# Performance work log

Hardware: AMD Instinct MI355X
Metric: run time of the kernel (lower is better)

## Reference

```python
import jax, jax.numpy as jnp
import numpy as np

B, P_LEN, Q_LEN, HID = 8, 2048, 1024, 1024


def setup_inputs() -> dict:
    key = jax.random.key(0)
    k1, k2, k3, k4 = jax.random.split(key, 4)
    k = jax.random.normal(k1, (B, P_LEN, HID), dtype=jnp.float32)
    q = jax.random.normal(k2, (B, Q_LEN, HID), dtype=jnp.float32)
    # q_mask: True = pad token. All-valid mask (no pads) to avoid NaN rows.
    q_mask = jnp.zeros((B, Q_LEN), dtype=bool)
    # Xavier-normal-initialized Linear weights, shape [out, in] as in torch.
    std = float(np.sqrt(2.0 / (HID + HID)))
    Wk = jax.random.normal(k3, (HID, HID), dtype=jnp.float32) * std
    Wq = jax.random.normal(k4, (HID, HID), dtype=jnp.float32) * std
    return {"k": k, "q": q, "q_mask": q_mask, "Wk": Wk, "Wq": Wq}


def reference(k, q, q_mask, Wk, Wq):
    # relu-projected keys/queries (Linear has no bias)
    p_key = jax.nn.relu(jnp.einsum('bpd,hd->bph', k, Wk))   # [B, p_len, hid]
    q_key = jax.nn.relu(jnp.einsum('bqd,hd->bqh', q, Wq))   # [B, q_len, hid]
    scores = jnp.einsum('bph,bqh->bpq', p_key, q_key)        # [B, p_len, q_len]
    scores = jnp.where(q_mask[:, None, :], -jnp.inf, scores)
    alphas = jax.nn.softmax(scores, axis=-1)                 # [B, p_len, q_len]
    ctx = jnp.einsum('bpq,bqd->bpd', alphas, q)              # [B, p_len, q_dim]
    return ctx, alphas
```

## Files before the change

### kernel.cpp

```cpp
#include <hip/hip_runtime.h>
#include <hip/hip_bf16.h>
#include <math.h>


typedef _Float16 v8h __attribute__((ext_vector_type(8)));
typedef _Float16 v4h __attribute__((ext_vector_type(4)));
typedef float v4f __attribute__((ext_vector_type(4)));

#define AS1C(p) ((const __attribute__((address_space(1))) void*)(p))
#define AS3(p)  ((__attribute__((address_space(3))) void*)(p))

__global__ __launch_bounds__(256) void gemm_nt_f16_128(
    const _Float16* __restrict__ A, const _Float16* __restrict__ B,
    float* __restrict__ Cf, _Float16* __restrict__ Ch,
    const _Float16* __restrict__ B2, _Float16* __restrict__ Ch2, int mtSplit,
    int N, int K, int Mtiles, int Ntiles,
    long long sA, long long sB, long long sC, int relu)
{
  extern __shared__ _Float16 lds[];

  const int nwg = gridDim.x;
  const int cpx = nwg >> 3;
  const int bid = (blockIdx.x & 7) * cpx + (blockIdx.x >> 3);
  const int nt  = bid % Ntiles;
  const int mt  = (bid / Ntiles) % Mtiles;
  const int bz  = bid / (Mtiles * Ntiles);

  A += (long long)bz * sA;

  const _Float16* Bp = B;
  _Float16* Chp = Ch;
  int m0c = mt * 128;
  if (mt >= mtSplit) { Bp = B2; Chp = Ch2; m0c = (mt - mtSplit) * 128; }
  Bp += (long long)bz * sB;

  const int m0g = mt * 128;
  const int n0  = nt * 128;
  const int t   = threadIdx.x;
  const int l   = t & 63;
  const int w   = t >> 6;
  const int wm  = (w >> 1) * 64;
  const int wn  = (w & 1) * 64;
  const int fr  = l & 15;
  const int fq  = l >> 4;
  const int r3  = fr & 7;
  const int sa0 = (fq ^ r3) * 8;
  const int sa1 = ((4 + fq) ^ r3) * 8;

  const int trow = t >> 3;
  const int tswz = ((t & 7) ^ (trow & 7)) * 8;

  const _Float16* Ast = A  + (long long)(m0g + trow) * K + tswz;
  const _Float16* Bst = Bp + (long long)(n0  + trow) * K + tswz;

  v4f acc[4][4];
#pragma unroll
  for (int i = 0; i < 4; ++i)
#pragma unroll
    for (int j = 0; j < 4; ++j)
      acc[i][j] = (v4f){0.f, 0.f, 0.f, 0.f};

  const int NT = K >> 6;

#define STAGE(kt) do {                                                                   \
    _Float16* s_ = lds + (((kt) & 1) << 14);                                             \
    const long long ko_ = (long long)((kt) << 6);                                        \
    __builtin_amdgcn_global_load_lds(AS1C(Ast + ko_),               AS3(s_ +        t * 8), 16, 0, 0); \
    __builtin_amdgcn_global_load_lds(AS1C(Ast + 32LL * K + ko_),    AS3(s_ + 2048 + t * 8), 16, 0, 0); \
    __builtin_amdgcn_global_load_lds(AS1C(Ast + 64LL * K + ko_),    AS3(s_ + 4096 + t * 8), 16, 0, 0); \
    __builtin_amdgcn_global_load_lds(AS1C(Ast + 96LL * K + ko_),    AS3(s_ + 6144 + t * 8), 16, 0, 0); \
    __builtin_amdgcn_global_load_lds(AS1C(Bst + ko_),               AS3(s_ + 8192 + t * 8), 16, 0, 0); \
    __builtin_amdgcn_global_load_lds(AS1C(Bst + 32LL * K + ko_),    AS3(s_ + 10240 + t * 8), 16, 0, 0); \
    __builtin_amdgcn_global_load_lds(AS1C(Bst + 64LL * K + ko_),    AS3(s_ + 12288 + t * 8), 16, 0, 0); \
    __builtin_amdgcn_global_load_lds(AS1C(Bst + 96LL * K + ko_),    AS3(s_ + 14336 + t * 8), 16, 0, 0); \
  } while (0)

  STAGE(0);

  for (int kt = 0; kt < NT; ++kt) {
    if (kt + 1 < NT) {
      STAGE(kt + 1);
      asm volatile("s_waitcnt vmcnt(8)" ::: "memory");
    } else {
      asm volatile("s_waitcnt vmcnt(0)" ::: "memory");
    }
    __builtin_amdgcn_sched_barrier(0);
    __builtin_amdgcn_s_barrier();
    asm volatile("" ::: "memory");

    const _Float16* Ab = lds + ((kt & 1) << 14);
    const _Float16* Bb = Ab + 8192;

    v8h a0[4], a1[4], b0[4], b1[4];

#pragma unroll
    for (int i = 0; i < 4; ++i) {
      a0[i] = *(const v8h*)&Ab[(wm + i * 16 + fr) * 64 + sa0];
      a1[i] = *(const v8h*)&Ab[(wm + i * 16 + fr) * 64 + sa1];
    }
#pragma unroll
    for (int j = 0; j < 2; ++j) {
      b0[j] = *(const v8h*)&Bb[(wn + j * 16 + fr) * 64 + sa0];
      b1[j] = *(const v8h*)&Bb[(wn + j * 16 + fr) * 64 + sa1];
    }
    __builtin_amdgcn_s_setprio(1);
#pragma unroll
    for (int i = 0; i < 4; ++i)
#pragma unroll
      for (int j = 0; j < 2; ++j) {
        acc[i][j] = __builtin_amdgcn_mfma_f32_16x16x32_f16(a0[i], b0[j], acc[i][j], 0, 0, 0);
        acc[i][j] = __builtin_amdgcn_mfma_f32_16x16x32_f16(a1[i], b1[j], acc[i][j], 0, 0, 0);
      }
    __builtin_amdgcn_s_setprio(0);

#pragma unroll
    for (int j = 2; j < 4; ++j) {
      b0[j] = *(const v8h*)&Bb[(wn + j * 16 + fr) * 64 + sa0];
      b1[j] = *(const v8h*)&Bb[(wn + j * 16 + fr) * 64 + sa1];
    }
    __builtin_amdgcn_s_setprio(1);
#pragma unroll
    for (int i = 0; i < 4; ++i)
#pragma unroll
      for (int j = 2; j < 4; ++j) {
        acc[i][j] = __builtin_amdgcn_mfma_f32_16x16x32_f16(a0[i], b0[j], acc[i][j], 0, 0, 0);
        acc[i][j] = __builtin_amdgcn_mfma_f32_16x16x32_f16(a1[i], b1[j], acc[i][j], 0, 0, 0);
      }
    __builtin_amdgcn_s_setprio(0);

    asm volatile("s_waitcnt lgkmcnt(0)" ::: "memory");
    __builtin_amdgcn_sched_barrier(0);
    __builtin_amdgcn_s_barrier();
  }
#undef STAGE

  float* Cfb = Cf ? Cf + (long long)bz * sC : nullptr;
  _Float16* Chb = Chp ? Chp + (long long)bz * sC : nullptr;
#pragma unroll
  for (int i = 0; i < 4; ++i) {
#pragma unroll
    for (int j = 0; j < 4; ++j) {
#pragma unroll
      for (int r = 0; r < 4; ++r) {
        const int row = m0c + wm + i * 16 + fq * 4 + r;
        const int col = n0 + wn + j * 16 + fr;
        float v = acc[i][j][r];
        if (relu) v = fmaxf(v, 0.f);
        if (Cfb) Cfb[(long long)row * N + col] = v;
        if (Chb) Chb[(long long)row * N + col] = (_Float16)v;
      }
    }
  }
}

__global__ __launch_bounds__(256) void convert_all_kernel(
    const float* __restrict__ s0, _Float16* __restrict__ d0, int b0,
    const float* __restrict__ s1, _Float16* __restrict__ d1, int b1,
    const float* __restrict__ s2, _Float16* __restrict__ d2, int b2,
    const float* __restrict__ s3, _Float16* __restrict__ d3)
{
  int blk = blockIdx.x;
  const float* src;
  _Float16* dst;
  if (blk < b0)           { src = s0; dst = d0; }
  else if (blk < b0 + b1) { src = s1; dst = d1; blk -= b0; }
  else if (blk < b0 + b1 + b2) { src = s2; dst = d2; blk -= b0 + b1; }
  else                    { src = s3; dst = d3; blk -= b0 + b1 + b2; }
  const long long i = ((long long)blk * 256 + threadIdx.x) * 4;
  const float4 v = *(const float4*)(src + i);
  v4h o = {(_Float16)v.x, (_Float16)v.y, (_Float16)v.z, (_Float16)v.w};
  *(v4h*)(dst + i) = o;
}

__global__ __launch_bounds__(256) void transpose_f16_kernel(
    const float* __restrict__ q, _Float16* __restrict__ qT, int Q, int H)
{
  __shared__ float tile[64][65];
  const float* qb = q + (long long)blockIdx.z * Q * H;
  _Float16* qTb = qT + (long long)blockIdx.z * H * Q;
  const int q0 = blockIdx.x * 64, h0 = blockIdx.y * 64;
  const int t = threadIdx.x;
  const int tr = t >> 4, tc = (t & 15) << 2;
#pragma unroll
  for (int i = 0; i < 4; ++i) {
    const float4 v = *(const float4*)(qb + (long long)(q0 + tr + i * 16) * H + h0 + tc);
    tile[tr + i * 16][tc + 0] = v.x;
    tile[tr + i * 16][tc + 1] = v.y;
    tile[tr + i * 16][tc + 2] = v.z;
    tile[tr + i * 16][tc + 3] = v.w;
  }
  __syncthreads();
#pragma unroll
  for (int i = 0; i < 4; ++i) {
    const int hl = tr + i * 16;
    const int ql = tc;
    v4h o = {(_Float16)tile[ql + 0][hl], (_Float16)tile[ql + 1][hl],
             (_Float16)tile[ql + 2][hl], (_Float16)tile[ql + 3][hl]};
    *(v4h*)(qTb + (long long)(h0 + hl) * Q + q0 + ql) = o;
  }
}

__global__ __launch_bounds__(256) void softmax_rows_kernel(
    float* __restrict__ S, _Float16* __restrict__ S16,
    const unsigned char* __restrict__ qmask, int Q, int P)
{
  const long long row = blockIdx.x;
  const int b = (int)(row / P);
  float* s = S + row * (long long)Q;
  const unsigned char* msk = qmask + (long long)b * Q;
  const int t = threadIdx.x;
  float4 v = *(const float4*)(s + (t << 2));
  float vals[4] = {v.x, v.y, v.z, v.w};
#pragma unroll
  for (int j = 0; j < 4; ++j)
    if (msk[(t << 2) + j]) vals[j] = -INFINITY;

  __shared__ float red[8];
  const int wid = t >> 6, lid = t & 63;

  float mx = fmaxf(fmaxf(vals[0], vals[1]), fmaxf(vals[2], vals[3]));
#pragma unroll
  for (int o = 32; o > 0; o >>= 1) mx = fmaxf(mx, __shfl_xor(mx, o, 64));
  if (lid == 0) red[wid] = mx;
  __syncthreads();
  mx = fmaxf(fmaxf(red[0], red[1]), fmaxf(red[2], red[3]));

  float e[4];
  float sum = 0.f;
#pragma unroll
  for (int j = 0; j < 4; ++j) { e[j] = __expf(vals[j] - mx); sum += e[j]; }
#pragma unroll
  for (int o = 32; o > 0; o >>= 1) sum += __shfl_xor(sum, o, 64);
  __syncthreads();
  if (lid == 0) red[4 + wid] = sum;
  __syncthreads();
  sum = red[4] + red[5] + red[6] + red[7];
  const float inv = 1.f / sum;

  float4 o;
  o.x = e[0] * inv; o.y = e[1] * inv; o.z = e[2] * inv; o.w = e[3] * inv;
  *(float4*)(s + (t << 2)) = o;
  v4h oh = {(_Float16)o.x, (_Float16)o.y, (_Float16)o.z, (_Float16)o.w};
  *(v4h*)(S16 + row * (long long)Q + (t << 2)) = oh;
}

extern "C" void kernel_launch(void* const* d_in, const int* in_sizes, int n_in,
                              void* d_out, int out_size, void* d_ws, size_t ws_size,
                              hipStream_t stream)
{
  const int B = 8, P = 2048, Q = 1024, H = 1024;
  const float* k  = (const float*)d_in[0];
  const float* q  = (const float*)d_in[1];
  const unsigned char* qmask = (const unsigned char*)d_in[2];
  const float* Wk = (const float*)d_in[3];
  const float* Wq = (const float*)d_in[4];

  float* ctx    = (float*)d_out;
  float* alphas = ctx + (size_t)B * P * H;

  _Float16* pkey16 = (_Float16*)d_out;

  char* wsb = (char*)d_ws;
  _Float16* qkey16   = (_Float16*)(wsb);
  _Float16* k16      = (_Float16*)(wsb + 16777216);
  _Float16* alphas16 = k16;
  _Float16* q16      = (_Float16*)(wsb + 16777216 + 33554432);
  _Float16* qT16     = q16;
  _Float16* Wk16     = (_Float16*)(wsb + 67108864);
  _Float16* Wq16     = (_Float16*)(wsb + 69206016);

  const long long nK = (long long)B * P * H;
  const long long nQ = (long long)B * Q * H;
  const long long nW = (long long)H * H;

  const int bK = (int)(nK / 1024), bQ = (int)(nQ / 1024), bW = (int)(nW / 1024);
  convert_all_kernel<<<bK + bQ + 2 * bW, 256, 0, stream>>>(
      k, k16, bK, q, q16, bQ, Wk, Wk16, bW, Wq, Wq16);

  const size_t LDSB = 65536;
  gemm_nt_f16_128<<<192 * 8, 256, LDSB, stream>>>(
      k16, Wk16, nullptr, pkey16, Wq16, qkey16, 128,
      H, H, 192, 8, 0LL, 0LL, 0LL, 1);
  gemm_nt_f16_128<<<16 * 8 * B, 256, LDSB, stream>>>(
      pkey16, qkey16, alphas, nullptr, qkey16, nullptr, 1 << 28,
      Q, H, 16, 8, (long long)P * H, (long long)Q * H, (long long)P * Q, 0);
  transpose_f16_kernel<<<dim3(Q / 64, H / 64, B), 256, 0, stream>>>(q, qT16, Q, H);
  softmax_rows_kernel<<<B * P, 256, 0, stream>>>(alphas, alphas16, qmask, Q, P);
  gemm_nt_f16_128<<<16 * 8 * B, 256, LDSB, stream>>>(
      alphas16, qT16, ctx, nullptr, qT16, nullptr, 1 << 28,
      H, Q, 16, 8, (long long)P * Q, (long long)H * Q, (long long)P * H, 0);
}
```

Measured before the change: 374.9 us.

## Enlarge GEMM tiles to 256x256 with 512 threads and split-stage prefetch

```diff
diff --git a/kernel.cpp b/kernel.cpp
--- a/kernel.cpp
+++ b/kernel.cpp
@@ -10,7 +10,7 @@
 #define AS1C(p) ((const __attribute__((address_space(1))) void*)(p))
 #define AS3(p)  ((__attribute__((address_space(3))) void*)(p))
 
-__global__ __launch_bounds__(256) void gemm_nt_f16_128(
+__global__ __launch_bounds__(512) void gemm_nt_f16_256(
     const _Float16* __restrict__ A, const _Float16* __restrict__ B,
     float* __restrict__ Cf, _Float16* __restrict__ Ch,
     const _Float16* __restrict__ B2, _Float16* __restrict__ Ch2, int mtSplit,
@@ -30,17 +30,17 @@
 
   const _Float16* Bp = B;
   _Float16* Chp = Ch;
-  int m0c = mt * 128;
-  if (mt >= mtSplit) { Bp = B2; Chp = Ch2; m0c = (mt - mtSplit) * 128; }
+  int m0c = mt * 256;
+  if (mt >= mtSplit) { Bp = B2; Chp = Ch2; m0c = (mt - mtSplit) * 256; }
   Bp += (long long)bz * sB;
 
-  const int m0g = mt * 128;
-  const int n0  = nt * 128;
+  const int m0g = mt * 256;
+  const int n0  = nt * 256;
   const int t   = threadIdx.x;
   const int l   = t & 63;
   const int w   = t >> 6;
-  const int wm  = (w >> 1) * 64;
-  const int wn  = (w & 1) * 64;
+  const int wm  = (w >> 2) * 128;
+  const int wn  = (w & 3) * 64;
   const int fr  = l & 15;
   const int fq  = l >> 4;
   const int r3  = fr & 7;
@@ -53,43 +53,34 @@
   const _Float16* Ast = A  + (long long)(m0g + trow) * K + tswz;
   const _Float16* Bst = Bp + (long long)(n0  + trow) * K + tswz;
 
-  v4f acc[4][4];
-#pragma unroll
-  for (int i = 0; i < 4; ++i)
+  v4f acc[8][4];
+#pragma unroll
+  for (int i = 0; i < 8; ++i)
 #pragma unroll
     for (int j = 0; j < 4; ++j)
       acc[i][j] = (v4f){0.f, 0.f, 0.f, 0.f};
 
   const int NT = K >> 6;
 
-#define STAGE(kt) do {                                                                   \
-    _Float16* s_ = lds + (((kt) & 1) << 14);                                             \
-    const long long ko_ = (long long)((kt) << 6);                                        \
-    __builtin_amdgcn_global_load_lds(AS1C(Ast + ko_),               AS3(s_ +        t * 8), 16, 0, 0); \
-    __builtin_amdgcn_global_load_lds(AS1C(Ast + 32LL * K + ko_),    AS3(s_ + 2048 + t * 8), 16, 0, 0); \
-    __builtin_amdgcn_global_load_lds(AS1C(Ast + 64LL * K + ko_),    AS3(s_ + 4096 + t * 8), 16, 0, 0); \
-    __builtin_amdgcn_global_load_lds(AS1C(Ast + 96LL * K + ko_),    AS3(s_ + 6144 + t * 8), 16, 0, 0); \
-    __builtin_amdgcn_global_load_lds(AS1C(Bst + ko_),               AS3(s_ + 8192 + t * 8), 16, 0, 0); \
-    __builtin_amdgcn_global_load_lds(AS1C(Bst + 32LL * K + ko_),    AS3(s_ + 10240 + t * 8), 16, 0, 0); \
-    __builtin_amdgcn_global_load_lds(AS1C(Bst + 64LL * K + ko_),    AS3(s_ + 12288 + t * 8), 16, 0, 0); \
-    __builtin_amdgcn_global_load_lds(AS1C(Bst + 96LL * K + ko_),    AS3(s_ + 14336 + t * 8), 16, 0, 0); \
+#define STAGE_HALF(kt, h) do {                                                            \
+    _Float16* s_ = lds + (((kt) & 1) * 32768) + (h) * 8192;                               \
+    const long long ko_ = (long long)((kt) << 6);                                         \
+    const long long ro_ = (long long)((h) * 128);                                         \
+    __builtin_amdgcn_global_load_lds(AS1C(Ast + ro_ * K + ko_),        AS3(s_ +         t * 8), 16, 0, 0); \
+    __builtin_amdgcn_global_load_lds(AS1C(Ast + (ro_ + 64) * K + ko_), AS3(s_ +  4096 + t * 8), 16, 0, 0); \
+    __builtin_amdgcn_global_load_lds(AS1C(Bst + ro_ * K + ko_),        AS3(s_ + 16384 + t * 8), 16, 0, 0); \
+    __builtin_amdgcn_global_load_lds(AS1C(Bst + (ro_ + 64) * K + ko_), AS3(s_ + 20480 + t * 8), 16, 0, 0); \
   } while (0)
 
-  STAGE(0);
+  STAGE_HALF(0, 0);
+  STAGE_HALF(0, 1);
+  asm volatile("s_waitcnt vmcnt(0)" ::: "memory");
+  __builtin_amdgcn_sched_barrier(0);
+  __builtin_amdgcn_s_barrier();
 
   for (int kt = 0; kt < NT; ++kt) {
-    if (kt + 1 < NT) {
-      STAGE(kt + 1);
-      asm volatile("s_waitcnt vmcnt(8)" ::: "memory");
-    } else {
-      asm volatile("s_waitcnt vmcnt(0)" ::: "memory");
-    }
-    __builtin_amdgcn_sched_barrier(0);
-    __builtin_amdgcn_s_barrier();
-    asm volatile("" ::: "memory");
-
-    const _Float16* Ab = lds + ((kt & 1) << 14);
-    const _Float16* Bb = Ab + 8192;
+    const _Float16* Ab = lds + ((kt & 1) * 32768);
+    const _Float16* Bb = Ab + 16384;
 
     v8h a0[4], a1[4], b0[4], b1[4];
 
@@ -103,6 +94,10 @@
       b0[j] = *(const v8h*)&Bb[(wn + j * 16 + fr) * 64 + sa0];
       b1[j] = *(const v8h*)&Bb[(wn + j * 16 + fr) * 64 + sa1];
     }
+    if (kt + 1 < NT) STAGE_HALF(kt + 1, 0);
+    __builtin_amdgcn_s_barrier();
+    asm volatile("s_waitcnt lgkmcnt(0)" ::: "memory");
+    __builtin_amdgcn_sched_barrier(0);
     __builtin_amdgcn_s_setprio(1);
 #pragma unroll
     for (int i = 0; i < 4; ++i)
@@ -112,12 +107,17 @@
         acc[i][j] = __builtin_amdgcn_mfma_f32_16x16x32_f16(a1[i], b1[j], acc[i][j], 0, 0, 0);
       }
     __builtin_amdgcn_s_setprio(0);
+    __builtin_amdgcn_s_barrier();
 
 #pragma unroll
     for (int j = 2; j < 4; ++j) {
       b0[j] = *(const v8h*)&Bb[(wn + j * 16 + fr) * 64 + sa0];
       b1[j] = *(const v8h*)&Bb[(wn + j * 16 + fr) * 64 + sa1];
     }
+    if (kt + 1 < NT) STAGE_HALF(kt + 1, 1);
+    __builtin_amdgcn_s_barrier();
+    asm volatile("s_waitcnt lgkmcnt(0)" ::: "memory");
+    __builtin_amdgcn_sched_barrier(0);
     __builtin_amdgcn_s_setprio(1);
 #pragma unroll
     for (int i = 0; i < 4; ++i)
@@ -127,17 +127,46 @@
         acc[i][j] = __builtin_amdgcn_mfma_f32_16x16x32_f16(a1[i], b1[j], acc[i][j], 0, 0, 0);
       }
     __builtin_amdgcn_s_setprio(0);
-
+    __builtin_amdgcn_s_barrier();
+
+#pragma unroll
+    for (int i = 0; i < 4; ++i) {
+      a0[i] = *(const v8h*)&Ab[(wm + 64 + i * 16 + fr) * 64 + sa0];
+      a1[i] = *(const v8h*)&Ab[(wm + 64 + i * 16 + fr) * 64 + sa1];
+    }
+    __builtin_amdgcn_s_barrier();
     asm volatile("s_waitcnt lgkmcnt(0)" ::: "memory");
     __builtin_amdgcn_sched_barrier(0);
+    __builtin_amdgcn_s_setprio(1);
+#pragma unroll
+    for (int i = 0; i < 4; ++i)
+#pragma unroll
+      for (int j = 2; j < 4; ++j) {
+        acc[4 + i][j] = __builtin_amdgcn_mfma_f32_16x16x32_f16(a0[i], b0[j], acc[4 + i][j], 0, 0, 0);
+        acc[4 + i][j] = __builtin_amdgcn_mfma_f32_16x16x32_f16(a1[i], b1[j], acc[4 + i][j], 0, 0, 0);
+      }
+    __builtin_amdgcn_s_setprio(0);
+    __builtin_amdgcn_s_barrier();
+
+    __builtin_amdgcn_s_setprio(1);
+#pragma unroll
+    for (int i = 0; i < 4; ++i)
+#pragma unroll
+      for (int j = 0; j < 2; ++j) {
+        acc[4 + i][j] = __builtin_amdgcn_mfma_f32_16x16x32_f16(a0[i], b0[j], acc[4 + i][j], 0, 0, 0);
+        acc[4 + i][j] = __builtin_amdgcn_mfma_f32_16x16x32_f16(a1[i], b1[j], acc[4 + i][j], 0, 0, 0);
+      }
+    __builtin_amdgcn_s_setprio(0);
+    asm volatile("s_waitcnt vmcnt(0)" ::: "memory");
+    __builtin_amdgcn_sched_barrier(0);
     __builtin_amdgcn_s_barrier();
   }
-#undef STAGE
+#undef STAGE_HALF
 
   float* Cfb = Cf ? Cf + (long long)bz * sC : nullptr;
   _Float16* Chb = Chp ? Chp + (long long)bz * sC : nullptr;
 #pragma unroll
-  for (int i = 0; i < 4; ++i) {
+  for (int i = 0; i < 8; ++i) {
 #pragma unroll
     for (int j = 0; j < 4; ++j) {
 #pragma unroll
@@ -277,16 +306,16 @@
   convert_all_kernel<<<bK + bQ + 2 * bW, 256, 0, stream>>>(
       k, k16, bK, q, q16, bQ, Wk, Wk16, bW, Wq, Wq16);
 
-  const size_t LDSB = 65536;
-  gemm_nt_f16_128<<<192 * 8, 256, LDSB, stream>>>(
-      k16, Wk16, nullptr, pkey16, Wq16, qkey16, 128,
-      H, H, 192, 8, 0LL, 0LL, 0LL, 1);
-  gemm_nt_f16_128<<<16 * 8 * B, 256, LDSB, stream>>>(
+  const size_t LDSB = 131072;
+  gemm_nt_f16_256<<<96 * 4, 512, LDSB, stream>>>(
+      k16, Wk16, nullptr, pkey16, Wq16, qkey16, 64,
+      H, H, 96, 4, 0LL, 0LL, 0LL, 1);
+  gemm_nt_f16_256<<<8 * 4 * B, 512, LDSB, stream>>>(
       pkey16, qkey16, alphas, nullptr, qkey16, nullptr, 1 << 28,
-      Q, H, 16, 8, (long long)P * H, (long long)Q * H, (long long)P * Q, 0);
+      Q, H, 8, 4, (long long)P * H, (long long)Q * H, (long long)P * Q, 0);
   transpose_f16_kernel<<<dim3(Q / 64, H / 64, B), 256, 0, stream>>>(q, qT16, Q, H);
   softmax_rows_kernel<<<B * P, 256, 0, stream>>>(alphas, alphas16, qmask, Q, P);
-  gemm_nt_f16_128<<<16 * 8 * B, 256, LDSB, stream>>>(
+  gemm_nt_f16_256<<<8 * 4 * B, 512, LDSB, stream>>>(
       alphas16, qT16, ctx, nullptr, qT16, nullptr, 1 << 28,
-      H, Q, 16, 8, (long long)P * Q, (long long)H * Q, (long long)P * H, 0);
-}
+      H, Q, 8, 4, (long long)P * Q, (long long)H * Q, (long long)P * H, 0);
+}
```

Measured after the change: 379.2 us. About the same (+1.1%).
